# Kernel tuning notes

Hardware: AMD Instinct MI355X
Metric: run time of the kernel (lower is better)

The kernel has to match this reference:

```python
import jax, jax.numpy as jnp
import numpy as np

B = 64        # number of tasks (sequential steps)
D = 512       # knowledge_representation_dim == understanding_representation_dim
M = 8192      # memory_slots
GAMMA = 0.95  # memory_gamma


def setup_inputs() -> dict:
    key = jax.random.key(0)
    k1, k2, k3, k4 = jax.random.split(key, 4)
    ortho = jax.nn.initializers.orthogonal()
    return {
        "k": jax.random.normal(k1, (B, 1, D), jnp.float32),
        "u": jax.random.normal(k2, (B, 1, D), jnp.float32),
        "memory_knowledge": ortho(k3, (D, M), jnp.float32),
        "memory_understanding": ortho(k4, (D, M), jnp.float32),
        "beta_param": jnp.float32(0.0),
        "memory_gamma": jnp.float32(GAMMA),
    }


def reference(k, u, memory_knowledge, memory_understanding, beta_param, memory_gamma):
    n_slots = memory_knowledge.shape[1]
    slot_ids = jnp.arange(n_slots)
    beta = jax.nn.sigmoid(beta_param)

    def step(carry, xs):
        MK, MU, w_w, w_u, w_lu = carry
        k_task, u_task = xs  # each [1, D]
        # cosine similarity of the task key against every memory column: [1, M]
        sim = (k_task @ MK) / (
            jnp.linalg.norm(k_task, axis=-1, keepdims=True)
            * jnp.linalg.norm(MK, axis=0, keepdims=True)
        )
        w_r = jax.nn.softmax(sim, axis=-1)[0]  # [M]
        # zero out the least-used slot (argmin of usage weights)
        keep = (slot_ids != jnp.argmin(w_u))[None, :]  # [1, M]
        MK = jnp.where(keep, MK, 0.0)
        MU = jnp.where(keep, MU, 0.0)
        # usage / write / least-used weight updates
        w_u = memory_gamma * w_u + w_r + w_w
        w_w = beta * jnp.mean(w_r) + (1.0 - beta) * w_lu  # [M] via broadcast of scalar mean
        w_lu = (slot_ids == jnp.argmin(w_u)).astype(MK.dtype)  # one-hot least-used
        # rank-1 write of understanding, then read refined understanding, then write knowledge
        MU = MU + u_task[0][:, None] * w_w[None, :]  # [D, M]
        u_ref = w_r @ MK.T  # [D] -- read uses MK after zeroing, before its write
        MK = MK + k_task[0][:, None] * w_w[None, :]  # [D, M]
        return (MK, MU, w_w, w_u, w_lu), u_ref

    zeros = jnp.zeros((n_slots,), memory_knowledge.dtype)
    init = (memory_knowledge, memory_understanding, zeros, zeros, zeros)
    _, u_refined = jax.lax.scan(step, init, (k, u))
    return u_refined[:, None, :]  # [B, 1, D]
```

## Files before the change

### kernel.cpp

```cpp
#include <hip/hip_runtime.h>
#include <math.h>

#define BB 64
#define DD 512
#define MM 8192
#define K2T 512
#define K2C 16

typedef unsigned long long u64;

template<int CTRL>
__device__ __forceinline__ float dpp_addf(float x) {
    int y = __builtin_amdgcn_update_dpp(0, __float_as_int(x), CTRL, 0xF, 0xF, true);
    return x + __int_as_float(y);
}
__device__ __forceinline__ float wave_sum64(float x) {
    x = dpp_addf<0x111>(x); x = dpp_addf<0x112>(x); x = dpp_addf<0x114>(x); x = dpp_addf<0x118>(x);
    x = dpp_addf<0x142>(x); x = dpp_addf<0x143>(x);
    return __int_as_float(__builtin_amdgcn_readlane(__float_as_int(x), 63));
}
__device__ __forceinline__ float readlane_f(float v, int l) {
    return __int_as_float(__builtin_amdgcn_readlane(__float_as_int(v), l));
}
template<int CTRL>
__device__ __forceinline__ u64 dpp_min_step(u64 k) {
    unsigned lo = (unsigned)k, hi = (unsigned)(k >> 32);
    unsigned nlo = (unsigned)__builtin_amdgcn_update_dpp((int)0xFFFFFFFFu, (int)lo, CTRL, 0xF, 0xF, false);
    unsigned nhi = (unsigned)__builtin_amdgcn_update_dpp((int)0xFFFFFFFFu, (int)hi, CTRL, 0xF, 0xF, false);
    u64 nk = (((u64)nhi) << 32) | (u64)nlo;
    return nk < k ? nk : k;
}
__device__ __forceinline__ u64 wave_min64_lane63(u64 k) {
    k = dpp_min_step<0x111>(k); k = dpp_min_step<0x112>(k); k = dpp_min_step<0x114>(k);
    k = dpp_min_step<0x118>(k); k = dpp_min_step<0x142>(k); k = dpp_min_step<0x143>(k);
    return k;
}
__device__ __forceinline__ u64 wave_min8(u64 k) {
    k = dpp_min_step<0x111>(k); k = dpp_min_step<0x112>(k); k = dpp_min_step<0x114>(k);
    unsigned lo = (unsigned)__builtin_amdgcn_readlane((int)(unsigned)k, 7);
    unsigned hi = (unsigned)__builtin_amdgcn_readlane((int)(unsigned)(k >> 32), 7);
    return (((u64)hi) << 32) | (u64)lo;
}

__device__ __forceinline__ void flag_release(int* p, int v) {
    __threadfence();
    __hip_atomic_store(p, v, __ATOMIC_RELEASE, __HIP_MEMORY_SCOPE_AGENT);
}
__device__ __forceinline__ void spin_until_eq(int* p, int want) {
    while (__hip_atomic_load(p, __ATOMIC_ACQUIRE, __HIP_MEMORY_SCOPE_AGENT) != want)
        __builtin_amdgcn_s_sleep(2);
}

struct K0Smem {
    float Ks[BB][129];
    float Gs[BB][BB];
};
struct KbSmem {
    float Ks[64 * 65];
    float Ms[64 * 65];
    float S0s[64 * 65];
    float sq[4 * 64];
    float n2A[64];
    float n2full[64];
    float Pfx0s[BB], invks[BB], k2s[BB];
};
#define KAB_SMEM ((sizeof(K0Smem) > sizeof(KbSmem)) ? sizeof(K0Smem) : sizeof(KbSmem))

__global__ __launch_bounds__(256) void kab_gram_ecold(const float* __restrict__ K,
                                                      const float* __restrict__ MK0,
                                                      const float* __restrict__ bp,
                                                      float* __restrict__ G, float* __restrict__ Pfx,
                                                      float* __restrict__ Ecold,
                                                      float* __restrict__ Spart,
                                                      int* __restrict__ flags) {
    __shared__ __align__(16) char blob[KAB_SMEM];
    const int tid = threadIdx.x;

    if (blockIdx.x == 0) {
        K0Smem* sm = (K0Smem*)blob;
        const int ti = ((tid >> 4) & 15) << 2;
        const int tj = (tid & 15) << 2;
        float acc[4][4];
        #pragma unroll
        for (int i = 0; i < 4; ++i)
            #pragma unroll
            for (int j = 0; j < 4; ++j) acc[i][j] = 0.f;
        for (int d0 = 0; d0 < DD; d0 += 128) {
            #pragma unroll
            for (int i = 0; i < 32; ++i) {
                int e = i * 256 + tid; int r = e >> 7, c = e & 127;
                sm->Ks[r][c] = K[r * DD + d0 + c];
            }
            __syncthreads();
            for (int dl = 0; dl < 128; ++dl) {
                float rv[4], cv[4];
                #pragma unroll
                for (int i = 0; i < 4; ++i) rv[i] = sm->Ks[ti + i][dl];
                #pragma unroll
                for (int j = 0; j < 4; ++j) cv[j] = sm->Ks[tj + j][dl];
                #pragma unroll
                for (int i = 0; i < 4; ++i)
                    #pragma unroll
                    for (int j = 0; j < 4; ++j) acc[i][j] += rv[i] * cv[j];
            }
            __syncthreads();
        }
        #pragma unroll
        for (int i = 0; i < 4; ++i)
            #pragma unroll
            for (int j = 0; j < 4; ++j) {
                G[(ti + i) * BB + tj + j] = acc[i][j];
                sm->Gs[ti + i][tj + j] = acc[i][j];
            }
        __syncthreads();
        const int s = tid & 63, w = tid >> 6;
        for (int rr = 0; rr < 16; ++rr) {
            int row = w * 16 + rr;
            float x = (s < row) ? sm->Gs[row][s] : 0.f;
            #pragma unroll
            for (int o = 1; o < 64; o <<= 1) {
                float y = __shfl_down(x, o);
                if (s + o < 64) x += y;
            }
            Pfx[row * BB + s] = x;
        }
        __syncthreads();
        if (tid == 0) flag_release(&flags[0], 1);
        return;
    }

    KbSmem* sm = (KbSmem*)blob;
    const int b = blockIdx.x - 1;
    const int lane = tid & 63, w = tid >> 6;
    const int jb = b * 64;
    const int t4 = ((w << 2) | (lane >> 4)) << 2;
    const int jq0 = lane & 15;

    float accA[4][4], accB[4][4];
    #pragma unroll
    for (int i = 0; i < 4; ++i)
        #pragma unroll
        for (int q = 0; q < 4; ++q) { accA[i][q] = 0.f; accB[i][q] = 0.f; }
    float sqaA = 0.f, sqaB = 0.f;
    for (int dt = 0; dt < 4; ++dt) {
        int d0 = dt * 64;
        #pragma unroll
        for (int i = 0; i < 16; ++i) {
            int e = i * 256 + tid; int r = e >> 6, c = e & 63;
            sm->Ks[r * 65 + c] = K[r * DD + d0 + c];
            float m = MK0[(d0 + r) * MM + jb + c];
            sm->Ms[r * 65 + c] = m;
            sqaA += m * m;
        }
        __syncthreads();
        #pragma unroll 4
        for (int dl = 0; dl < 64; ++dl) {
            float kv[4], mv[4];
            #pragma unroll
            for (int i = 0; i < 4; ++i) kv[i] = sm->Ks[(t4 + i) * 65 + dl];
            #pragma unroll
            for (int q = 0; q < 4; ++q) mv[q] = sm->Ms[dl * 65 + jq0 + 16 * q];
            #pragma unroll
            for (int i = 0; i < 4; ++i)
                #pragma unroll
                for (int q = 0; q < 4; ++q) accA[i][q] += kv[i] * mv[q];
        }
        __syncthreads();
    }
    for (int dt = 0; dt < 4; ++dt) {
        int d0 = 256 + dt * 64;
        #pragma unroll
        for (int i = 0; i < 16; ++i) {
            int e = i * 256 + tid; int r = e >> 6, c = e & 63;
            sm->Ks[r * 65 + c] = K[r * DD + d0 + c];
            float m = MK0[(d0 + r) * MM + jb + c];
            sm->Ms[r * 65 + c] = m;
            sqaB += m * m;
        }
        __syncthreads();
        #pragma unroll 4
        for (int dl = 0; dl < 64; ++dl) {
            float kv[4], mv[4];
            #pragma unroll
            for (int i = 0; i < 4; ++i) kv[i] = sm->Ks[(t4 + i) * 65 + dl];
            #pragma unroll
            for (int q = 0; q < 4; ++q) mv[q] = sm->Ms[dl * 65 + jq0 + 16 * q];
            #pragma unroll
            for (int i = 0; i < 4; ++i)
                #pragma unroll
                for (int q = 0; q < 4; ++q) accB[i][q] += kv[i] * mv[q];
        }
        __syncthreads();
    }
    sm->sq[w * 64 + lane] = sqaA;
    __syncthreads();
    if (w == 0) sm->n2A[lane] = sm->sq[lane] + sm->sq[64 + lane] + sm->sq[128 + lane] + sm->sq[192 + lane];
    __syncthreads();
    sm->sq[w * 64 + lane] = sqaB;
    __syncthreads();
    if (w == 0) {
        float b4 = sm->sq[lane] + sm->sq[64 + lane] + sm->sq[128 + lane] + sm->sq[192 + lane];
        sm->n2full[lane] = sm->n2A[lane] + b4;
    }
    #pragma unroll
    for (int i = 0; i < 4; ++i)
        #pragma unroll
        for (int q = 0; q < 4; ++q)
            sm->S0s[(t4 + i) * 65 + jq0 + 16 * q] = accA[i][q] + accB[i][q];
    if (tid == 0) spin_until_eq(&flags[0], 1);
    __syncthreads();
    if (tid < BB) {
        float g = G[tid * BB + tid];
        sm->k2s[tid] = g;
        sm->invks[tid] = __builtin_amdgcn_rsqf(g);
        sm->Pfx0s[tid] = Pfx[tid * BB + 0];
    }
    __syncthreads();
    if (w == 0) {
        const float beta = 1.f / (1.f + expf(-bp[0]));
        const float cuni = beta / (float)MM;
        int j = jb + lane;
        float n2c = sm->n2full[lane];
        for (int t = 0; t < BB; ++t) {
            float s0 = sm->S0s[t * 65 + lane];
            float d_ = s0 + cuni * sm->Pfx0s[t];
            float cosv = d_ * sm->invks[t] * __builtin_amdgcn_rsqf(n2c);
            float ee = __expf(cosv);
            Ecold[t * MM + j] = ee;
            float rs = wave_sum64(ee);
            if (lane == 0) Spart[t * 128 + b] = rs;
            n2c = n2c + 2.f * cuni * d_ + cuni * cuni * sm->k2s[t];
        }
    }
}

struct ScanSmem {
    u64   red[2][8];
    float EtabL[BB * BB];
    float EcTabL[BB * BB];
    float invSL[BB];
    float SL[BB];
    int   endL[BB];
    float invS_bc[2];
};
struct K3Smem {
    float Ws[64 * 65];
    float Msub[64 * 65];
};
struct K4Smem {
    float Arow[BB];
    float Drow[BB];
    int   hcs[BB];
};
#define SM3 ((sizeof(ScanSmem) > sizeof(K3Smem)) ? sizeof(ScanSmem) : sizeof(K3Smem))
#define SMEM_BYTES ((SM3 > sizeof(K4Smem)) ? SM3 : sizeof(K4Smem))

__global__ __launch_bounds__(512) void k23_mega(const float* __restrict__ Ecold,
                                                const float* __restrict__ G,
                                                const float* __restrict__ Pfx,
                                                const float* __restrict__ Spart,
                                                const float* __restrict__ bp,
                                                const float* __restrict__ gp,
                                                const float* __restrict__ MK0,
                                                const float* __restrict__ K,
                                                float* __restrict__ Etab_g,
                                                float* __restrict__ EcTab_g,
                                                float* __restrict__ Sg,
                                                float* __restrict__ invSg,
                                                int*   __restrict__ endTab_g,
                                                int*   __restrict__ hcolg,
                                                float* __restrict__ parts,
                                                float* __restrict__ out,
                                                int*   __restrict__ flags) {
    __shared__ __align__(16) char smem_raw[SMEM_BYTES];
    const int tid = threadIdx.x;
    const int bx = blockIdx.x;

    if (bx >= 1 && bx <= 256) {
        K3Smem* sm = (K3Smem*)smem_raw;
        const int tile = bx - 1;
        const int d0 = (tile & 7) * 64;
        const int by = tile >> 3;
        const bool act = tid < 256;
        const int lane = tid & 63, w = tid >> 6;
        const int t4 = ((w << 2) | (lane >> 4)) << 2;
        const int dq0 = lane & 15;
        float acc[4][4];
        #pragma unroll
        for (int i = 0; i < 4; ++i)
            #pragma unroll
            for (int q = 0; q < 4; ++q) acc[i][q] = 0.f;
        for (int sub = 0; sub < 4; ++sub) {
            int jb = by * 256 + sub * 64;
            if (act) {
                #pragma unroll
                for (int i = 0; i < 16; ++i) {
                    int e = i * 256 + tid; int r = e >> 6, c = e & 63;
                    sm->Ws[r * 65 + c] = Ecold[r * MM + jb + c];
                    sm->Msub[r * 65 + c] = MK0[(d0 + r) * MM + jb + c];
                }
            }
            __syncthreads();
            if (act) {
                #pragma unroll 4
                for (int jl = 0; jl < 64; ++jl) {
                    float wv[4], mv[4];
                    #pragma unroll
                    for (int i = 0; i < 4; ++i) wv[i] = sm->Ws[(t4 + i) * 65 + jl];
                    #pragma unroll
                    for (int q = 0; q < 4; ++q) mv[q] = sm->Msub[(dq0 + 16 * q) * 65 + jl];
                    #pragma unroll
                    for (int i = 0; i < 4; ++i)
                        #pragma unroll
                        for (int q = 0; q < 4; ++q) acc[i][q] += wv[i] * mv[q];
                }
            }
            __syncthreads();
        }
        if (act) {
            #pragma unroll
            for (int i = 0; i < 4; ++i)
                #pragma unroll
                for (int q = 0; q < 4; ++q)
                    parts[(by * 64 + t4 + i) * DD + d0 + dq0 + 16 * q] = acc[i][q];
        }
        __syncthreads();
        if (tid == 0) { __threadfence(); atomicAdd(&flags[2], 1); }
        return;
    }

    if (bx >= 257) {
        K4Smem* sm = (K4Smem*)smem_raw;
        const int t = bx - 257;
        const int d = tid;
        if (tid == 0) {
            spin_until_eq(&flags[1], 1);
            while (__hip_atomic_load(&flags[2], __ATOMIC_ACQUIRE, __HIP_MEMORY_SCOPE_AGENT) < 256)
                __builtin_amdgcn_s_sleep(2);
        }
        __syncthreads();
        if (d < BB) {
            sm->hcs[d] = hcolg[d];
            const float beta = 1.f / (1.f + expf(-bp[0]));
            const float cuni = beta / (float)MM;
            const float omb  = 1.f - beta;
            int s = d;
            float Ev = Etab_g[t * BB + s];
            int endv = endTab_g[s];
            bool act = (s <= t) && (t < endv);
            float S = Sg[t], invS = invSg[t];
            float ev = act ? Ev : 0.f;
            float x = ev;
            #pragma unroll
            for (int o = 1; o < 64; o <<= 1) {
                float y = __shfl_down(x, o);
                if (s + o < 64) x += y;
            }
            float suf = x - ev;
            float arow = 0.f;
            if (s < t) {
                float Qe = S - suf;
                arow = cuni * Qe;
                if (s >= 1 && act) arow += omb * Ev;
                arow *= invS;
            }
            sm->Arow[s] = arow;
            sm->Drow[s] = act ? (-invS * EcTab_g[t * BB + s]) : 0.f;
        }
        __syncthreads();
        float isv = invSg[t];
        float s1 = 0.f;
        #pragma unroll
        for (int p = 0; p < 32; ++p) s1 += parts[(p * 64 + t) * DD + d];
        float s2 = 0.f;
        for (int i = 0; i < BB; ++i) s2 += sm->Drow[i] * MK0[d * MM + sm->hcs[i]];
        float s3 = 0.f;
        for (int i = 0; i < BB; ++i) s3 += sm->Arow[i] * K[i * DD + d];
        out[t * DD + d] = isv * s1 + s2 + s3;
        return;
    }

    ScanSmem* sm = (ScanSmem*)smem_raw;
    const int lane = tid & 63;
    const int wid = tid >> 6;
    const bool w0 = (wid == 0);

    const float beta  = 1.f / (1.f + expf(-bp[0]));
    const float gamma = gp[0];
    const float cuni  = beta / (float)MM;
    const float omb   = 1.f - beta;

    if (tid < BB) sm->endL[tid] = BB;

    const float4* Ec4 = reinterpret_cast<const float4*>(Ecold);

    float wu[K2C], e0[K2C], e1[K2C], e2[K2C];
    #pragma unroll
    for (int c = 0; c < K2C; ++c) wu[c] = 0.f;
    #pragma unroll
    for (int i = 0; i < K2C / 4; ++i) {
        float4 v = Ec4[i * K2T + tid];
        e0[4 * i + 0] = v.x; e0[4 * i + 1] = v.y; e0[4 * i + 2] = v.z; e0[4 * i + 3] = v.w;
        float4 u = Ec4[(MM / 4) + i * K2T + tid];
        e1[4 * i + 0] = u.x; e1[4 * i + 1] = u.y; e1[4 * i + 2] = u.z; e1[4 * i + 3] = u.w;
    }

    float scold_r = 0.f;
    if (w0) {
        const float4* sp4 = reinterpret_cast<const float4*>(Spart + lane * 128);
        float sc = 0.f;
        #pragma unroll 8
        for (int i = 0; i < 32; ++i) {
            float4 v = sp4[i];
            sc += v.x; sc += v.y; sc += v.z; sc += v.w;
        }
        scold_r = sc;
    }

    float slot_n2 = 0.f, slot_ec = 0.f, wu_hot = 0.f, e_true_c = 0.f;
    int   slot_j = -1;
    bool  slot_act = false;
    float k2_cur = 0.f, S_reg = 0.f, invS_reg = 0.f;

    if (w0) {
        float g0 = G[lane];
        k2_cur = readlane_f(g0, 0);
        S_reg = readlane_f(scold_r, 0);
        invS_reg = __builtin_amdgcn_rcpf(S_reg);
        if (lane == 0) sm->invS_bc[0] = invS_reg;
    }
    __syncthreads();

    auto step = [&](int t, float (&cur)[K2C], float (&ld)[K2C]) {
        float grow_n = 0.f, pfx_n = 0.f, Ssc_n = 0.f, ecpf0 = 0.f;
        if (w0 && t + 1 < BB) {
            if (slot_act) ecpf0 = Ecold[(t + 1) * MM + slot_j];
            grow_n = G[(t + 1) * BB + lane];
            pfx_n  = Pfx[(t + 1) * BB + lane];
            Ssc_n  = readlane_f(scold_r, t + 1);
        }

        int j0; float minval;
        if (t == 0) { j0 = 0; minval = 0.f; }
        else {
            u64 pm = sm->red[t & 1][lane & 7];
            pm = wave_min8(pm);
            j0 = (int)(pm & 0xFFFFFFFFu);
            minval = __uint_as_float((unsigned)(pm >> 32));
        }
        const float cuni_t = (t == 0) ? 0.f : cuni;
        float invS = w0 ? invS_reg : sm->invS_bc[t & 1];

        float latev = 0.f, ecpf_t = 0.f;
        if (w0 && lane == t) {
            latev = Ecold[t * MM + j0];
            if (t + 1 < BB) ecpf_t = Ecold[(t + 1) * MM + j0];
        }
        __builtin_amdgcn_sched_barrier(0);
        if (t + 2 < BB) {
            #pragma unroll
            for (int i = 0; i < K2C / 4; ++i) {
                float4 v = Ec4[(t + 2) * (MM / 4) + i * K2T + tid];
                ld[4 * i + 0] = v.x; ld[4 * i + 1] = v.y; ld[4 * i + 2] = v.z; ld[4 * i + 3] = v.w;
            }
        }
        __builtin_amdgcn_sched_barrier(0);

        bool fresh = false;
        if (w0) {
            u64 sup = __ballot(slot_act && (slot_j == j0));
            const bool has_sup = (sup != 0ull);
            const int  ssup = has_sup ? (int)__builtin_ctzll(sup) : 0;

            if (slot_act) {
                float ww = cuni + ((t >= 2 && lane == t - 1) ? omb : 0.f);
                wu_hot = fmaf(gamma, wu_hot, fmaf(e_true_c, invS, ww));
            }
            float trans_wu = readlane_f(wu_hot, ssup);
            float trans_E  = readlane_f(e_true_c, ssup);

            if (lane == t) {
                slot_j = j0;
                float ww0 = cuni + ((t >= 1) ? omb : 0.f);
                slot_n2 = ww0 * ww0 * k2_cur;
                slot_act = true;
                if (has_sup) wu_hot = trans_wu;
                fresh = !has_sup;
            }
            if (has_sup) {
                if (lane == ssup) slot_act = false;
                if (lane == t) sm->endL[ssup] = t;
            }

            float etl = e_true_c, ecl = slot_ec;
            if (lane == t) { ecl = latev; etl = has_sup ? trans_E : latev; }
            sm->EtabL[t * BB + lane]  = etl;
            sm->EcTabL[t * BB + lane] = ecl;
            if (lane == 0) { sm->invSL[t] = invS; sm->SL[t] = S_reg; }

            if (fresh) wu_hot = fmaf(gamma, minval, fmaf(latev, invS, cuni_t));

            if (t + 1 < BB) {
                float d_ = cuni * pfx_n;
                if (lane >= 1) d_ += omb * grow_n;
                float k2n   = readlane_f(grow_n, t + 1);
                float invkn = __builtin_amdgcn_rsqf(k2n);
                float ecpf  = (lane == t) ? ecpf_t : ecpf0;
                float myDelta = 0.f;
                float e_n = 0.f;
                if (slot_act) {
                    e_n = __expf(d_ * invkn * __builtin_amdgcn_rsqf(slot_n2));
                    myDelta = e_n - ecpf;
                    slot_n2 = slot_n2 + 2.f * cuni * d_ + cuni * cuni * k2n;
                }
                float S_next = Ssc_n + wave_sum64(myDelta);
                float invS_next = __builtin_amdgcn_rcpf(S_next);
                if (lane == 0) sm->invS_bc[(t + 1) & 1] = invS_next;
                if (slot_act) slot_ec = ecpf;
                e_true_c = e_n;
                k2_cur = k2n;
                S_reg = S_next; invS_reg = invS_next;
            }
        }

        float vmin = 0.f; int jmin = 0;
        #pragma unroll
        for (int i = 0; i < 4; ++i) {
            #pragma unroll
            for (int q = 0; q < 4; ++q) {
                int c = i * 4 + q;
                float wun = fmaf(gamma, wu[c], fmaf(cur[c], invS, cuni_t));
                wu[c] = wun;
                int j = i * 2048 + (tid << 2) + q;
                if (c == 0) { vmin = wun; jmin = j; }
                else if (wun < vmin) { vmin = wun; jmin = j; }
            }
        }
        u64 key = (((u64)__float_as_uint(vmin)) << 32) | (unsigned)jmin;

        if (((j0 >> 2) & (K2T - 1)) == tid) {
            int cj = ((j0 >> 11) << 2) | (j0 & 3);
            #pragma unroll
            for (int c = 0; c < K2C; ++c) if (c == cj) wu[c] = __builtin_inff();
        }

        if (w0) {
            u64 skey = (slot_act && !fresh)
                     ? ((((u64)__float_as_uint(wu_hot)) << 32) | (unsigned)slot_j) : ~0ull;
            key = skey < key ? skey : key;
        }
        key = wave_min64_lane63(key);
        if (lane == 63) sm->red[(t + 1) & 1][wid] = key;

        asm volatile("s_waitcnt lgkmcnt(0)" ::: "memory");
        __builtin_amdgcn_s_barrier();
        asm volatile("" ::: "memory");
    };

    #pragma unroll 1
    for (int th = 0; th < 63; th += 3) {
        step(th + 0, e0, e2);
        step(th + 1, e1, e0);
        step(th + 2, e2, e1);
    }
    step(63, e0, e2);

    for (int i = tid; i < BB * BB; i += K2T) {
        Etab_g[i]  = sm->EtabL[i];
        EcTab_g[i] = sm->EcTabL[i];
    }
    if (tid < BB) {
        Sg[tid] = sm->SL[tid];
        invSg[tid] = sm->invSL[tid];
        endTab_g[tid] = sm->endL[tid];
    }
    if (w0) hcolg[lane] = slot_j;
    __syncthreads();
    if (tid == 0) flag_release(&flags[1], 1);
}

extern "C" void kernel_launch(void* const* d_in, const int* in_sizes, int n_in,
                              void* d_out, int out_size, void* d_ws, size_t ws_size,
                              hipStream_t stream) {
    const float* K   = (const float*)d_in[0];
    const float* MK0 = (const float*)d_in[2];
    const float* bp  = (const float*)d_in[4];
    const float* gp  = (const float*)d_in[5];

    float* ws    = (float*)d_ws;
    float* G     = ws;
    float* Pfx   = G + 4096;
    float* Ecold = Pfx + 4096;
    float* Spart = Ecold + 524288;
    float* Etab  = Spart + 8192;
    float* EcTab = Etab + 4096;
    float* Sarr  = EcTab + 4096;
    float* invS  = Sarr + 64;
    float* parts = invS + 64;
    int*   hcol  = (int*)(parts + 1048576);
    int*   endT  = hcol + 64;
    int*   flags = endT + 64;
    float* out   = (float*)d_out;

    hipMemsetAsync(flags, 0, 3 * sizeof(int), stream);
    kab_gram_ecold <<<129, 256, 0, stream>>>(K, MK0, bp, G, Pfx, Ecold, Spart, flags);
    k23_mega       <<<321, 512, 0, stream>>>(Ecold, G, Pfx, Spart, bp, gp, MK0, K,
                                             Etab, EcTab, Sarr, invS, endT, hcol, parts, out, flags);
}
```

Measured before the change: 257.8 us.

## Split mega-kernel into scan/GEMM, gather and final kernels without spin flags

```diff
diff --git a/kernel.cpp b/kernel.cpp
--- a/kernel.cpp
+++ b/kernel.cpp
@@ -243,48 +243,41 @@
     int   endL[BB];
     float invS_bc[2];
 };
-struct K3Smem {
+struct K3Smem2 {
     float Ws[64 * 65];
-    float Msub[64 * 65];
+    float MsubA[64 * 65];
+    float MsubB[64 * 65];
 };
-struct K4Smem {
-    float Arow[BB];
-    float Drow[BB];
-    int   hcs[BB];
-};
-#define SM3 ((sizeof(ScanSmem) > sizeof(K3Smem)) ? sizeof(ScanSmem) : sizeof(K3Smem))
-#define SMEM_BYTES ((SM3 > sizeof(K4Smem)) ? SM3 : sizeof(K4Smem))
-
-__global__ __launch_bounds__(512) void k23_mega(const float* __restrict__ Ecold,
-                                                const float* __restrict__ G,
-                                                const float* __restrict__ Pfx,
-                                                const float* __restrict__ Spart,
-                                                const float* __restrict__ bp,
-                                                const float* __restrict__ gp,
-                                                const float* __restrict__ MK0,
-                                                const float* __restrict__ K,
-                                                float* __restrict__ Etab_g,
-                                                float* __restrict__ EcTab_g,
-                                                float* __restrict__ Sg,
-                                                float* __restrict__ invSg,
-                                                int*   __restrict__ endTab_g,
-                                                int*   __restrict__ hcolg,
-                                                float* __restrict__ parts,
-                                                float* __restrict__ out,
-                                                int*   __restrict__ flags) {
+#define SMEM_BYTES ((sizeof(ScanSmem) > sizeof(K3Smem2)) ? sizeof(ScanSmem) : sizeof(K3Smem2))
+
+__global__ __launch_bounds__(512) void k23_scan_u1(const float* __restrict__ Ecold,
+                                                   const float* __restrict__ G,
+                                                   const float* __restrict__ Pfx,
+                                                   const float* __restrict__ Spart,
+                                                   const float* __restrict__ bp,
+                                                   const float* __restrict__ gp,
+                                                   const float* __restrict__ MK0,
+                                                   float* __restrict__ Etab_g,
+                                                   float* __restrict__ EcTab_g,
+                                                   float* __restrict__ Sg,
+                                                   float* __restrict__ invSg,
+                                                   int*   __restrict__ endTab_g,
+                                                   int*   __restrict__ hcolg,
+                                                   float* __restrict__ parts) {
     __shared__ __align__(16) char smem_raw[SMEM_BYTES];
     const int tid = threadIdx.x;
-    const int bx = blockIdx.x;
-
-    if (bx >= 1 && bx <= 256) {
-        K3Smem* sm = (K3Smem*)smem_raw;
-        const int tile = bx - 1;
-        const int d0 = (tile & 7) * 64;
-        const int by = tile >> 3;
-        const bool act = tid < 256;
-        const int lane = tid & 63, w = tid >> 6;
+
+    if (blockIdx.x != 0) {
+        K3Smem2* sm = (K3Smem2*)smem_raw;
+        const int p = blockIdx.x - 1;
+        const int by = p >> 2;
+        const int half = tid >> 8;
+        const int g = tid & 255;
+        const int d0 = (p & 3) * 128 + half * 64;
+        const int lane = g & 63, w = g >> 6;
         const int t4 = ((w << 2) | (lane >> 4)) << 2;
         const int dq0 = lane & 15;
+        float* Msub = half ? sm->MsubB : sm->MsubA;
         float acc[4][4];
         #pragma unroll
         for (int i = 0; i < 4; ++i)
@@ -292,91 +285,40 @@
             for (int q = 0; q < 4; ++q) acc[i][q] = 0.f;
         for (int sub = 0; sub < 4; ++sub) {
             int jb = by * 256 + sub * 64;
-            if (act) {
+            if (half == 0) {
                 #pragma unroll
                 for (int i = 0; i < 16; ++i) {
-                    int e = i * 256 + tid; int r = e >> 6, c = e & 63;
+                    int e = i * 256 + g; int r = e >> 6, c = e & 63;
                     sm->Ws[r * 65 + c] = Ecold[r * MM + jb + c];
-                    sm->Msub[r * 65 + c] = MK0[(d0 + r) * MM + jb + c];
+                    sm->MsubA[r * 65 + c] = MK0[(d0 + r) * MM + jb + c];
                 }
+            } else {
+                #pragma unroll
+                for (int i = 0; i < 16; ++i) {
+                    int e = i * 256 + g; int r = e >> 6, c = e & 63;
+                    sm->MsubB[r * 65 + c] = MK0[(d0 + r) * MM + jb + c];
+                }
             }
             __syncthreads();
-            if (act) {
-                #pragma unroll 4
-                for (int jl = 0; jl < 64; ++jl) {
-                    float wv[4], mv[4];
+            #pragma unroll 4
+            for (int jl = 0; jl < 64; ++jl) {
+                float wv[4], mv[4];
+                #pragma unroll
+                for (int i = 0; i < 4; ++i) wv[i] = sm->Ws[(t4 + i) * 65 + jl];
+                #pragma unroll
+                for (int q = 0; q < 4; ++q) mv[q] = Msub[(dq0 + 16 * q) * 65 + jl];
+                #pragma unroll
+                for (int i = 0; i < 4; ++i)
                     #pragma unroll
-                    for (int i = 0; i < 4; ++i) wv[i] = sm->Ws[(t4 + i) * 65 + jl];
-                    #pragma unroll
-                    for (int q = 0; q < 4; ++q) mv[q] = sm->Msub[(dq0 + 16 * q) * 65 + jl];
-                    #pragma unroll
-                    for (int i = 0; i < 4; ++i)
-                        #pragma unroll
-                        for (int q = 0; q < 4; ++q) acc[i][q] += wv[i] * mv[q];
-                }
+                    for (int q = 0; q < 4; ++q) acc[i][q] += wv[i] * mv[q];
             }
             __syncthreads();
         }
-        if (act) {
-            #pragma unroll
-            for (int i = 0; i < 4; ++i)
-                #pragma unroll
-                for (int q = 0; q < 4; ++q)
-                    parts[(by * 64 + t4 + i) * DD + d0 + dq0 + 16 * q] = acc[i][q];
-        }
-        __syncthreads();
-        if (tid == 0) { __threadfence(); atomicAdd(&flags[2], 1); }
-        return;
-    }
-
-    if (bx >= 257) {
-        K4Smem* sm = (K4Smem*)smem_raw;
-        const int t = bx - 257;
-        const int d = tid;
-        if (tid == 0) {
-            spin_until_eq(&flags[1], 1);
-            while (__hip_atomic_load(&flags[2], __ATOMIC_ACQUIRE, __HIP_MEMORY_SCOPE_AGENT) < 256)
-                __builtin_amdgcn_s_sleep(2);
-        }
-        __syncthreads();
-        if (d < BB) {
-            sm->hcs[d] = hcolg[d];
-            const float beta = 1.f / (1.f + expf(-bp[0]));
-            const float cuni = beta / (float)MM;
-            const float omb  = 1.f - beta;
-            int s = d;
-            float Ev = Etab_g[t * BB + s];
-            int endv = endTab_g[s];
-            bool act = (s <= t) && (t < endv);
-            float S = Sg[t], invS = invSg[t];
-            float ev = act ? Ev : 0.f;
-            float x = ev;
-            #pragma unroll
-            for (int o = 1; o < 64; o <<= 1) {
-                float y = __shfl_down(x, o);
-                if (s + o < 64) x += y;
-            }
-            float suf = x - ev;
-            float arow = 0.f;
-            if (s < t) {
-                float Qe = S - suf;
-                arow = cuni * Qe;
-                if (s >= 1 && act) arow += omb * Ev;
-                arow *= invS;
-            }
-            sm->Arow[s] = arow;
-            sm->Drow[s] = act ? (-invS * EcTab_g[t * BB + s]) : 0.f;
-        }
-        __syncthreads();
-        float isv = invSg[t];
-        float s1 = 0.f;
-        #pragma unroll
-        for (int p = 0; p < 32; ++p) s1 += parts[(p * 64 + t) * DD + d];
-        float s2 = 0.f;
-        for (int i = 0; i < BB; ++i) s2 += sm->Drow[i] * MK0[d * MM + sm->hcs[i]];
-        float s3 = 0.f;
-        for (int i = 0; i < BB; ++i) s3 += sm->Arow[i] * K[i * DD + d];
-        out[t * DD + d] = isv * s1 + s2 + s3;
+        #pragma unroll
+        for (int i = 0; i < 4; ++i)
+            #pragma unroll
+            for (int q = 0; q < 4; ++q)
+                parts[(by * 64 + t4 + i) * DD + d0 + dq0 + 16 * q] = acc[i][q];
         return;
     }
 
@@ -575,8 +517,65 @@
         endTab_g[tid] = sm->endL[tid];
     }
     if (w0) hcolg[lane] = slot_j;
+}
+
+__global__ __launch_bounds__(512) void k3b_gather(const float* __restrict__ MK0, const int* __restrict__ hcolg,
+                                                  float* __restrict__ MKhot) {
+    int i = blockIdx.x, d = threadIdx.x;
+    int h = hcolg[i];
+    MKhot[i * DD + d] = MK0[d * MM + h];
+}
+
+__global__ __launch_bounds__(512) void k4_final(const float* __restrict__ parts,
+                                                const float* __restrict__ K,
+                                                const float* __restrict__ Etab,
+                                                const float* __restrict__ EcTab,
+                                                const int*   __restrict__ endTab,
+                                                const float* __restrict__ Sg,
+                                                const float* __restrict__ invSg,
+                                                const float* __restrict__ MKhot,
+                                                const float* __restrict__ bp,
+                                                float* __restrict__ out) {
+    __shared__ float Arow[BB];
+    __shared__ float Drow[BB];
+    int t = blockIdx.x, d = threadIdx.x;
+    if (d < BB) {
+        const float beta = 1.f / (1.f + expf(-bp[0]));
+        const float cuni = beta / (float)MM;
+        const float omb  = 1.f - beta;
+        int s = d;
+        float Ev = Etab[t * BB + s];
+        int endv = endTab[s];
+        bool act = (s <= t) && (t < endv);
+        float S = Sg[t], invS = invSg[t];
+        float ev = act ? Ev : 0.f;
+        float x = ev;
+        #pragma unroll
+        for (int o = 1; o < 64; o <<= 1) {
+            float y = __shfl_down(x, o);
+            if (s + o < 64) x += y;
+        }
+        float suf = x - ev;
+        float arow = 0.f;
+        if (s < t) {
+            float Qe = S - suf;
+            arow = cuni * Qe;
+            if (s >= 1 && act) arow += omb * Ev;
+            arow *= invS;
+        }
+        Arow[s] = arow;
+        Drow[s] = act ? (-invS * EcTab[t * BB + s]) : 0.f;
+    }
     __syncthreads();
-    if (tid == 0) flag_release(&flags[1], 1);
+    float isv = invSg[t];
+    float s1 = 0.f;
+    #pragma unroll
+    for (int p = 0; p < 32; ++p) s1 += parts[(p * 64 + t) * DD + d];
+    float s2 = 0.f;
+    for (int i = 0; i < BB; ++i) s2 += Drow[i] * MKhot[i * DD + d];
+    float s3 = 0.f;
+    for (int i = 0; i < BB; ++i) s3 += Arow[i] * K[i * DD + d];
+    out[t * DD + d] = isv * s1 + s2 + s3;
 }
 
 extern "C" void kernel_launch(void* const* d_in, const int* in_sizes, int n_in,
@@ -596,14 +595,17 @@
     float* EcTab = Etab + 4096;
     float* Sarr  = EcTab + 4096;
     float* invS  = Sarr + 64;
-    float* parts = invS + 64;
+    float* MKhot = invS + 64;
+    float* parts = MKhot + 32768;
     int*   hcol  = (int*)(parts + 1048576);
     int*   endT  = hcol + 64;
     int*   flags = endT + 64;
     float* out   = (float*)d_out;
 
-    hipMemsetAsync(flags, 0, 3 * sizeof(int), stream);
+    hipMemsetAsync(flags, 0, sizeof(int), stream);
     kab_gram_ecold <<<129, 256, 0, stream>>>(K, MK0, bp, G, Pfx, Ecold, Spart, flags);
-    k23_mega       <<<321, 512, 0, stream>>>(Ecold, G, Pfx, Spart, bp, gp, MK0, K,
-                                             Etab, EcTab, Sarr, invS, endT, hcol, parts, out, flags);
-}
+    k23_scan_u1    <<<129, 512, 0, stream>>>(Ecold, G, Pfx, Spart, bp, gp, MK0,
+                                             Etab, EcTab, Sarr, invS, endT, hcol, parts);
+    k3b_gather     <<<64, 512, 0, stream>>>(MK0, hcol, MKhot);
+    k4_final       <<<64, 512, 0, stream>>>(parts, K, Etab, EcTab, endT, Sarr, invS, MKhot, bp, out);
+}
```

Measured after the change: 214.6 us. 1.2x faster.
